# Performance work log

Hardware: AMD Instinct MI355X
Metric: run time of the kernel (lower is better)

## Reference

```python
import jax, jax.numpy as jnp
import numpy as np

EPS = 1e-5
NUM_HEADS = 8
KEY_DIM = 16
D = 64  # attn_ratio * key_dim


def conv1x1_bn(x, w, g, b, m, v):
    # x: (B, Cin, H, W), w: (Cout, Cin); eval-mode BatchNorm over channel dim
    y = jnp.einsum('bchw,oc->bohw', x, w)
    scale = (g * jax.lax.rsqrt(v + EPS))[None, :, None, None]
    shift = (b - g * m * jax.lax.rsqrt(v + EPS))[None, :, None, None]
    return y * scale + shift


def setup_inputs() -> dict:
    key = jax.random.key(0)
    ks = jax.random.split(key, 22)
    dim, nh_kd, dh = 384, 128, 512
    f = jax.random.normal
    u = jax.random.uniform
    return {
        'x': f(ks[0], (2, dim, 56, 56), jnp.float32),
        'wq': f(ks[1], (nh_kd, dim), jnp.float32) * 0.05,
        'qg': u(ks[2], (nh_kd,), jnp.float32), 'qb': f(ks[3], (nh_kd,)) * 0.1,
        'qm': f(ks[4], (nh_kd,)) * 0.1, 'qv': u(ks[5], (nh_kd,)) + 0.5,
        'wk': f(ks[6], (nh_kd, dim), jnp.float32) * 0.05,
        'kg': u(ks[7], (nh_kd,), jnp.float32), 'kb': f(ks[8], (nh_kd,)) * 0.1,
        'km': f(ks[9], (nh_kd,)) * 0.1, 'kvv': u(ks[10], (nh_kd,)) + 0.5,
        'wv': f(ks[11], (dh, dim), jnp.float32) * 0.05,
        'vg': u(ks[12], (dh,), jnp.float32), 'vb': f(ks[13], (dh,)) * 0.1,
        'vm': f(ks[14], (dh,)) * 0.1, 'vvv': u(ks[15], (dh,)) + 0.5,
        'wp': f(ks[16], (dim, dh), jnp.float32) * 0.05,
        'pg': u(ks[17], (dim,), jnp.float32), 'pb': f(ks[18], (dim,)) * 0.1,
        'pm': f(ks[19], (dim,)) * 0.1, 'pvv': u(ks[20], (dim,)) + 0.5,
    }


def reference(x, wq, qg, qb, qm, qv, wk, kg, kb, km, kvv,
              wv, vg, vb, vm, vvv, wp, pg, pb, pm, pvv):
    B, C, H, W = x.shape
    N = H * W
    h, kd, d = NUM_HEADS, KEY_DIM, D
    # (B, h, N, kd)
    qq = conv1x1_bn(x, wq, qg, qb, qm, qv).reshape(B, h, kd, N).transpose(0, 1, 3, 2)
    # (B, h, kd, N)
    kk = conv1x1_bn(x, wk, kg, kb, km, kvv).reshape(B, h, kd, N)
    # (B, h, N, d)
    vv = conv1x1_bn(x, wv, vg, vb, vm, vvv).reshape(B, h, d, N).transpose(0, 1, 3, 2)
    # NOTE: original forward does NOT apply self.scale
    attn = jax.nn.softmax(jnp.matmul(qq, kk), axis=-1)  # (B, h, N, N)
    xx = jnp.matmul(attn, vv)                            # (B, h, N, d)
    xx = xx.transpose(0, 1, 3, 2).reshape(B, h * d, H, W)
    xx = jax.nn.relu(xx)
    return conv1x1_bn(xx, wp, pg, pb, pm, pvv)
```

## Files before the change

kernel.cpp:

```cpp
#include <hip/hip_runtime.h>
#include <hip/hip_bf16.h>

#define B_   2
#define CIN  384
#define NPIX 3136
#define NH   8
#define KD   16
#define DHEAD 64
#define NHKD 128
#define QKW  256
#define DHD  512
#define EPSW 1e-5f

typedef __attribute__((ext_vector_type(8))) short vshort8;
typedef __attribute__((ext_vector_type(4))) short vshort4;
typedef __attribute__((ext_vector_type(4))) float vfloat4;

static __device__ __forceinline__ float bf2f(short s) {
    unsigned int u = ((unsigned int)(unsigned short)s) << 16;
    return __builtin_bit_cast(float, u);
}
static __device__ __forceinline__ short f2bf(float f) {
    unsigned int u = __builtin_bit_cast(unsigned int, f);
    unsigned int lsb = (u >> 16) & 1u;
    u += 0x7fffu + lsb;
    return (short)(u >> 16);
}
static __device__ __forceinline__ float pget(const void* p, int i, int f32) {
    return f32 ? ((const float*)p)[i] : bf2f(((const short*)p)[i]);
}

__global__ void detect_dtype(const unsigned short* __restrict__ x, int* __restrict__ flag) {
    int lane = threadIdx.x & 63;
    int cnt = 0;
#pragma unroll
    for (int j = 0; j < 8; j++) {
        int e = (x[(lane * 8 + j) * 2] >> 7) & 0xFF;
        cnt += (e >= 0xC0);
    }
    cnt += __shfl_xor(cnt, 1);
    cnt += __shfl_xor(cnt, 2);
    cnt += __shfl_xor(cnt, 4);
    cnt += __shfl_xor(cnt, 8);
    cnt += __shfl_xor(cnt, 16);
    cnt += __shfl_xor(cnt, 32);
    if (threadIdx.x == 0) *flag = (cnt >= 16) ? 1 : 0;
}

__global__ __launch_bounds__(256) void convert_and_bn(
    const void* __restrict__ wq, const void* __restrict__ wk,
    const void* __restrict__ wv, const void* __restrict__ wp,
    short* __restrict__ wB,
    const void* qg, const void* qb, const void* qm, const void* qv,
    const void* kg, const void* kb, const void* km, const void* kv,
    const void* vg, const void* vb, const void* vm, const void* vv,
    const void* pg, const void* pb, const void* pm, const void* pv,
    float* __restrict__ scA, float* __restrict__ shA,
    const int* __restrict__ flag)
{
    int f32 = *flag;
    int i = blockIdx.x * 256 + threadIdx.x;
    {
        const void* src; int j;
        if (i < 49152)       { src = wq; j = i; }
        else if (i < 98304)  { src = wk; j = i - 49152; }
        else if (i < 294912) { src = wv; j = i - 98304; }
        else                 { src = wp; j = i - 294912; }
        wB[i] = f32 ? f2bf(((const float*)src)[j]) : ((const short*)src)[j];
    }
    if (i < 1152) {
        const void *g, *bb, *mn, *vr; int j;
        if (i < 128)      { g = qg; bb = qb; mn = qm; vr = qv; j = i; }
        else if (i < 256) { g = kg; bb = kb; mn = km; vr = kv; j = i - 128; }
        else if (i < 768) { g = vg; bb = vb; mn = vm; vr = vv; j = i - 256; }
        else              { g = pg; bb = pb; mn = pm; vr = pv; j = i - 768; }
        float iv = rsqrtf(pget(vr, j, f32) + EPSW);
        float s = pget(g, j, f32) * iv;
        scA[i] = s;
        shA[i] = pget(bb, j, f32) - pget(mn, j, f32) * s;
    }
}

__global__ __launch_bounds__(256) void transpose_k(const void* __restrict__ x,
                                                   short* __restrict__ xT,
                                                   const int* __restrict__ flag) {
    __shared__ short tile[32][33];
    int f32 = *flag;
    int b = blockIdx.z, n0 = blockIdx.x * 32, c0 = blockIdx.y * 32;
    int t = threadIdx.x;
    int r = t >> 3, q4 = (t & 7) * 4;
    size_t off = ((size_t)b * CIN + c0 + r) * NPIX + n0 + q4;
    if (f32) {
        float4 v = *(const float4*)((const float*)x + off);
        tile[r][q4 + 0] = f2bf(v.x);
        tile[r][q4 + 1] = f2bf(v.y);
        tile[r][q4 + 2] = f2bf(v.z);
        tile[r][q4 + 3] = f2bf(v.w);
    } else {
        vshort4 v = *(const vshort4*)((const short*)x + off);
#pragma unroll
        for (int i = 0; i < 4; i++) tile[r][q4 + i] = v[i];
    }
    __syncthreads();
    vshort4 o;
#pragma unroll
    for (int i = 0; i < 4; i++) o[i] = tile[q4 + i][r];
    *(vshort4*)(xT + ((size_t)b * NPIX + n0 + r) * CIN + c0 + q4) = o;
}

__global__ __launch_bounds__(256) void gemm_bt_bn(
    const short* __restrict__ A, long sAb,
    const short* __restrict__ Bt, long sBb,
    void* __restrict__ C, long sCb,
    const float* __restrict__ sc, const float* __restrict__ sh,
    int Nb, int K, int bnPerRow, int finalOut,
    const int* __restrict__ flag)
{
    __shared__ __attribute__((aligned(16))) short Al[64 * 72];
    __shared__ __attribute__((aligned(16))) short Bl[64 * 72];
    int f32 = finalOut ? *flag : 0;
    int b = blockIdx.z;
    const short* Ab = A + (size_t)b * sAb;
    const short* Bb = Bt + (size_t)b * sBb;
    size_t cbase = (size_t)b * sCb;
    int m0 = blockIdx.x * 64, n0 = blockIdx.y * 64;
    int t = threadIdx.x, lane = t & 63, w = t >> 6, m = lane & 15, quad = lane >> 4;
    int srow = t >> 2, scol = (t & 3) * 16;
    const short* ag = Ab + (size_t)(m0 + srow) * K + scol;
    const short* bg = Bb + (size_t)(n0 + srow) * K + scol;
    vfloat4 acc[4];
#pragma unroll
    for (int i = 0; i < 4; i++) acc[i] = (vfloat4){0.f, 0.f, 0.f, 0.f};

    for (int k0 = 0; k0 < K; k0 += 64) {
        vshort8 a0 = *(const vshort8*)(ag + k0);
        vshort8 a1 = *(const vshort8*)(ag + k0 + 8);
        vshort8 b0 = *(const vshort8*)(bg + k0);
        vshort8 b1 = *(const vshort8*)(bg + k0 + 8);
        __syncthreads();
        *(vshort8*)&Al[srow * 72 + scol] = a0;
        *(vshort8*)&Al[srow * 72 + scol + 8] = a1;
        *(vshort8*)&Bl[srow * 72 + scol] = b0;
        *(vshort8*)&Bl[srow * 72 + scol + 8] = b1;
        __syncthreads();
#pragma unroll
        for (int kk = 0; kk < 2; kk++) {
            vshort8 af = *(const vshort8*)&Al[(w * 16 + m) * 72 + kk * 32 + quad * 8];
#pragma unroll
            for (int nc = 0; nc < 4; nc++) {
                vshort8 bf = *(const vshort8*)&Bl[(nc * 16 + m) * 72 + kk * 32 + quad * 8];
                acc[nc] = __builtin_amdgcn_mfma_f32_16x16x32_bf16(af, bf, acc[nc], 0, 0, 0);
            }
        }
    }

#pragma unroll
    for (int nc = 0; nc < 4; nc++) {
        int col = n0 + nc * 16 + m;
        float scc = bnPerRow ? 0.f : sc[col];
        float shc = bnPerRow ? 0.f : sh[col];
#pragma unroll
        for (int r = 0; r < 4; r++) {
            int row = m0 + w * 16 + quad * 4 + r;
            float s2 = bnPerRow ? sc[row] : scc;
            float h2 = bnPerRow ? sh[row] : shc;
            float val = s2 * acc[nc][r] + h2;
            size_t idx = cbase + (size_t)row * Nb + col;
            if (finalOut && f32) ((float*)C)[idx] = val;
            else                 ((short*)C)[idx] = f2bf(val);
        }
    }
}

__global__ __launch_bounds__(256) void attn_kernel(
    const short* __restrict__ QKt, const short* __restrict__ V,
    short* __restrict__ xx)
{
    __shared__ __attribute__((aligned(16))) short Kl[2][64 * 40];
    __shared__ __attribute__((aligned(16))) short Vl[2][64 * 72];
    __shared__ __attribute__((aligned(16))) short Pl[64 * 72];
    int bh = blockIdx.y, b = bh >> 3, h = bh & 7;
    int q0 = blockIdx.x * 64;
    int t = threadIdx.x, lane = t & 63, w = t >> 6, m = lane & 15, quad = lane >> 4;

    {
        int key = t >> 2;
        int z = 16 + (t & 3) * 4;
        *(vshort4*)&Kl[0][key * 40 + z] = (vshort4){0, 0, 0, 0};
        *(vshort4*)&Kl[1][key * 40 + z] = (vshort4){0, 0, 0, 0};
    }

    int q = q0 + w * 16 + m;
    vshort8 aq;
    if (quad < 2) {
        aq = *(const vshort8*)(QKt + ((size_t)b * NPIX + q) * QKW + h * KD + quad * 8);
    } else {
        aq = (vshort8){0, 0, 0, 0, 0, 0, 0, 0};
    }

    vfloat4 o[4], o4;
#pragma unroll
    for (int i = 0; i < 4; i++) o[i] = (vfloat4){0.f, 0.f, 0.f, 0.f};
    o4 = (vfloat4){0.f, 0.f, 0.f, 0.f};

    int skey = t >> 2, skd = (t & 3) * 4;
    const short* kgp = QKt + (size_t)b * NPIX * QKW + NHKD + h * KD + skd;
    int vrow = t >> 2, vcol = (t & 3) * 16;
    const short* vgp = V + ((size_t)(b * DHD) + h * DHEAD + vrow) * NPIX + vcol;
    const vfloat4 zero4 = (vfloat4){0.f, 0.f, 0.f, 0.f};
    const short one_bf = (short)0x3F80;
    const vshort8 ones = {one_bf, one_bf, one_bf, one_bf, one_bf, one_bf, one_bf, one_bf};

    {
        vshort4 kstg = *(const vshort4*)(kgp + (size_t)skey * QKW);
        vshort8 v0 = *(const vshort8*)(vgp);
        vshort8 v1 = *(const vshort8*)(vgp + 8);
        *(vshort4*)&Kl[0][skey * 40 + skd] = kstg;
        *(vshort8*)&Vl[0][vrow * 72 + vcol] = v0;
        *(vshort8*)&Vl[0][vrow * 72 + vcol + 8] = v1;
    }
    __syncthreads();

    for (int it = 0; it < NPIX / 64; ++it) {
        int cur = it & 1, nxt = cur ^ 1;
        int k0 = it * 64;
        int more = (it + 1) < (NPIX / 64);
        vshort4 kstg; vshort8 v0, v1;
        if (more) {
            kstg = *(const vshort4*)(kgp + (size_t)(k0 + 64 + skey) * QKW);
            v0 = *(const vshort8*)(vgp + k0 + 64);
            v1 = *(const vshort8*)(vgp + k0 + 72);
        }

        vfloat4 s[4];
#pragma unroll
        for (int c = 0; c < 4; c++) {
            vshort8 ak = *(const vshort8*)&Kl[cur][(c * 16 + m) * 40 + quad * 8];
            s[c] = __builtin_amdgcn_mfma_f32_16x16x32_bf16(ak, aq, zero4, 0, 0, 0);
        }

        short* pw = &Pl[(w * 16 + m) * 72];
#pragma unroll
        for (int c = 0; c < 4; c++) {
            vshort4 pv;
#pragma unroll
            for (int r = 0; r < 4; r++) {
                float p = __expf(s[c][r]);
                pv[r] = (short)(__builtin_bit_cast(unsigned int, p) >> 16);
            }
            *(vshort4*)&pw[c * 16 + quad * 4] = pv;
        }

#pragma unroll
        for (int kc = 0; kc < 2; kc++) {
            vshort8 ap = *(const vshort8*)&Pl[(w * 16 + m) * 72 + kc * 32 + quad * 8];
#pragma unroll
            for (int dc = 0; dc < 4; dc++) {
                vshort8 bv = *(const vshort8*)&Vl[cur][(dc * 16 + m) * 72 + kc * 32 + quad * 8];
                o[dc] = __builtin_amdgcn_mfma_f32_16x16x32_bf16(ap, bv, o[dc], 0, 0, 0);
            }
            o4 = __builtin_amdgcn_mfma_f32_16x16x32_bf16(ap, ones, o4, 0, 0, 0);
        }

        if (more) {
            *(vshort4*)&Kl[nxt][skey * 40 + skd] = kstg;
            *(vshort8*)&Vl[nxt][vrow * 72 + vcol] = v0;
            *(vshort8*)&Vl[nxt][vrow * 72 + vcol + 8] = v1;
        }
        __syncthreads();
    }

#pragma unroll
    for (int r = 0; r < 4; r++) {
        float inv = 1.0f / o4[r];
        int qrow = q0 + w * 16 + quad * 4 + r;
        size_t base = ((size_t)b * NPIX + qrow) * DHD + h * DHEAD + m;
#pragma unroll
        for (int dc = 0; dc < 4; dc++) {
            float val = o[dc][r] * inv;
            val = fmaxf(val, 0.0f);
            xx[base + dc * 16] = f2bf(val);
        }
    }
}

extern "C" void kernel_launch(void* const* d_in, const int* in_sizes, int n_in,
                              void* d_out, int out_size, void* d_ws, size_t ws_size,
                              hipStream_t stream) {
    const void* x  = d_in[0];
    const void* wq = d_in[1];
    const void* qg = d_in[2];  const void* qb = d_in[3];
    const void* qm = d_in[4];  const void* qv = d_in[5];
    const void* wk = d_in[6];
    const void* kg = d_in[7];  const void* kb = d_in[8];
    const void* km = d_in[9];  const void* kv = d_in[10];
    const void* wv = d_in[11];
    const void* vg = d_in[12]; const void* vb = d_in[13];
    const void* vm = d_in[14]; const void* vv = d_in[15];
    const void* wp = d_in[16];
    const void* pg = d_in[17]; const void* pb = d_in[18];
    const void* pm = d_in[19]; const void* pv = d_in[20];

    short* xT  = (short*)d_ws;
    short* wB  = xT + (size_t)B_ * NPIX * CIN;
    short* wqkB = wB;
    short* wvB  = wB + 98304;
    short* wpB  = wB + 294912;
    short* QKt = wB + 491520;
    short* Vb  = QKt + (size_t)B_ * NPIX * QKW;
    short* xx  = Vb + (size_t)B_ * DHD * NPIX;
    float* scA = (float*)(xx + (size_t)B_ * NPIX * DHD);
    float* shA = scA + 1152;
    int* flag  = (int*)(shA + 1152);

    detect_dtype<<<1, 64, 0, stream>>>((const unsigned short*)x, flag);
    convert_and_bn<<<491520 / 256, 256, 0, stream>>>(
        wq, wk, wv, wp, wB,
        qg, qb, qm, qv, kg, kb, km, kv,
        vg, vb, vm, vv, pg, pb, pm, pv, scA, shA, flag);
    transpose_k<<<dim3(NPIX / 32, CIN / 32, B_), 256, 0, stream>>>(x, xT, flag);

    gemm_bt_bn<<<dim3(NPIX / 64, QKW / 64, B_), 256, 0, stream>>>(
        xT, (long)NPIX * CIN, wqkB, 0, QKt, (long)NPIX * QKW,
        scA, shA, QKW, CIN, 0, 0, flag);
    gemm_bt_bn<<<dim3(DHD / 64, NPIX / 64, B_), 256, 0, stream>>>(
        wvB, 0, xT, (long)NPIX * CIN, Vb, (long)DHD * NPIX,
        scA + 256, shA + 256, NPIX, CIN, 1, 0, flag);

    attn_kernel<<<dim3(NPIX / 64, B_ * NH), 256, 0, stream>>>(QKt, Vb, xx);

    gemm_bt_bn<<<dim3(CIN / 64, NPIX / 64, B_), 256, 0, stream>>>(
        wpB, 0, xx, (long)NPIX * DHD, d_out, (long)CIN * NPIX,
        scA + 768, shA + 768, NPIX, DHD, 1, 1, flag);
}
```

Baseline: 214.0 us.

## Fuse prep and projection launches, switch attention to 32x32 MFMA tiles

Folds dtype detection, weight conversion, BN folding and the input transpose into one prep kernel, and merges the QK and V projection GEMMs into a single launch, cutting the launch count from seven to four. The attention kernel now uses 128-thread blocks with two waves of 32 queries each and 32x32x16 bf16 MFMAs. This removes the zero-padded K tile the old kernel needed to fit the 16-wide key dim into 16x16x32. Every block now recomputes the dtype detection redundantly, and fewer waves per block may lower latency hiding in attention.

```diff
diff --git a/kernel.cpp b/kernel.cpp
--- a/kernel.cpp
+++ b/kernel.cpp
@@ -15,6 +15,7 @@
 typedef __attribute__((ext_vector_type(8))) short vshort8;
 typedef __attribute__((ext_vector_type(4))) short vshort4;
 typedef __attribute__((ext_vector_type(4))) float vfloat4;
+typedef __attribute__((ext_vector_type(16))) float vfloat16;
 
 static __device__ __forceinline__ float bf2f(short s) {
     unsigned int u = ((unsigned int)(unsigned short)s) << 16;
@@ -30,64 +31,59 @@
     return f32 ? ((const float*)p)[i] : bf2f(((const short*)p)[i]);
 }
 
-__global__ void detect_dtype(const unsigned short* __restrict__ x, int* __restrict__ flag) {
+static __device__ __forceinline__ int detect_f32(const unsigned short* x) {
     int lane = threadIdx.x & 63;
-    int cnt = 0;
+    bool big = false;
 #pragma unroll
     for (int j = 0; j < 8; j++) {
         int e = (x[(lane * 8 + j) * 2] >> 7) & 0xFF;
-        cnt += (e >= 0xC0);
-    }
-    cnt += __shfl_xor(cnt, 1);
-    cnt += __shfl_xor(cnt, 2);
-    cnt += __shfl_xor(cnt, 4);
-    cnt += __shfl_xor(cnt, 8);
-    cnt += __shfl_xor(cnt, 16);
-    cnt += __shfl_xor(cnt, 32);
-    if (threadIdx.x == 0) *flag = (cnt >= 16) ? 1 : 0;
-}
-
-__global__ __launch_bounds__(256) void convert_and_bn(
+        big = big || (e >= 0xC0);
+    }
+    unsigned long long bal = __ballot(big);
+    return __popcll(bal) >= 32;
+}
+
+__global__ __launch_bounds__(256) void prep_kernel(
+    const void* __restrict__ x,
     const void* __restrict__ wq, const void* __restrict__ wk,
     const void* __restrict__ wv, const void* __restrict__ wp,
-    short* __restrict__ wB,
+    short* __restrict__ wB, short* __restrict__ xT,
     const void* qg, const void* qb, const void* qm, const void* qv,
     const void* kg, const void* kb, const void* km, const void* kv,
     const void* vg, const void* vb, const void* vm, const void* vv,
     const void* pg, const void* pb, const void* pm, const void* pv,
-    float* __restrict__ scA, float* __restrict__ shA,
-    const int* __restrict__ flag)
-{
-    int f32 = *flag;
-    int i = blockIdx.x * 256 + threadIdx.x;
-    {
+    float* __restrict__ scA, float* __restrict__ shA)
+{
+    __shared__ short tile[32][33];
+    int f32 = detect_f32((const unsigned short*)x);
+    int id = blockIdx.x;
+    int t = threadIdx.x;
+
+    if (id < 1920) {
+        int i = id * 256 + t;
         const void* src; int j;
         if (i < 49152)       { src = wq; j = i; }
         else if (i < 98304)  { src = wk; j = i - 49152; }
         else if (i < 294912) { src = wv; j = i - 98304; }
         else                 { src = wp; j = i - 294912; }
         wB[i] = f32 ? f2bf(((const float*)src)[j]) : ((const short*)src)[j];
-    }
-    if (i < 1152) {
-        const void *g, *bb, *mn, *vr; int j;
-        if (i < 128)      { g = qg; bb = qb; mn = qm; vr = qv; j = i; }
-        else if (i < 256) { g = kg; bb = kb; mn = km; vr = kv; j = i - 128; }
-        else if (i < 768) { g = vg; bb = vb; mn = vm; vr = vv; j = i - 256; }
-        else              { g = pg; bb = pb; mn = pm; vr = pv; j = i - 768; }
-        float iv = rsqrtf(pget(vr, j, f32) + EPSW);
-        float s = pget(g, j, f32) * iv;
-        scA[i] = s;
-        shA[i] = pget(bb, j, f32) - pget(mn, j, f32) * s;
-    }
-}
-
-__global__ __launch_bounds__(256) void transpose_k(const void* __restrict__ x,
-                                                   short* __restrict__ xT,
-                                                   const int* __restrict__ flag) {
-    __shared__ short tile[32][33];
-    int f32 = *flag;
-    int b = blockIdx.z, n0 = blockIdx.x * 32, c0 = blockIdx.y * 32;
-    int t = threadIdx.x;
+        if (i < 1152) {
+            const void *g, *bb, *mn, *vr;
+            if (i < 128)      { g = qg; bb = qb; mn = qm; vr = qv; j = i; }
+            else if (i < 256) { g = kg; bb = kb; mn = km; vr = kv; j = i - 128; }
+            else if (i < 768) { g = vg; bb = vb; mn = vm; vr = vv; j = i - 256; }
+            else              { g = pg; bb = pb; mn = pm; vr = pv; j = i - 768; }
+            float iv = rsqrtf(pget(vr, j, f32) + EPSW);
+            float s = pget(g, j, f32) * iv;
+            scA[i] = s;
+            shA[i] = pget(bb, j, f32) - pget(mn, j, f32) * s;
+        }
+        return;
+    }
+
+    int tid2 = id - 1920;
+    int b = tid2 / 1176, rr = tid2 % 1176;
+    int n0 = (rr % 98) * 32, c0 = (rr / 98) * 32;
     int r = t >> 3, q4 = (t & 7) * 4;
     size_t off = ((size_t)b * CIN + c0 + r) * NPIX + n0 + q4;
     if (f32) {
@@ -108,26 +104,17 @@
     *(vshort4*)(xT + ((size_t)b * NPIX + n0 + r) * CIN + c0 + q4) = o;
 }
 
-__global__ __launch_bounds__(256) void gemm_bt_bn(
-    const short* __restrict__ A, long sAb,
-    const short* __restrict__ Bt, long sBb,
-    void* __restrict__ C, long sCb,
+static __device__ __forceinline__ void gemm_body(
+    short* Al, short* Bl,
+    const short* __restrict__ A, const short* __restrict__ Bt,
+    void* __restrict__ C, size_t coff, int m0, int n0,
     const float* __restrict__ sc, const float* __restrict__ sh,
-    int Nb, int K, int bnPerRow, int finalOut,
-    const int* __restrict__ flag)
-{
-    __shared__ __attribute__((aligned(16))) short Al[64 * 72];
-    __shared__ __attribute__((aligned(16))) short Bl[64 * 72];
-    int f32 = finalOut ? *flag : 0;
-    int b = blockIdx.z;
-    const short* Ab = A + (size_t)b * sAb;
-    const short* Bb = Bt + (size_t)b * sBb;
-    size_t cbase = (size_t)b * sCb;
-    int m0 = blockIdx.x * 64, n0 = blockIdx.y * 64;
+    int Nb, int K, int bnPerRow, int finalOut, int f32)
+{
     int t = threadIdx.x, lane = t & 63, w = t >> 6, m = lane & 15, quad = lane >> 4;
     int srow = t >> 2, scol = (t & 3) * 16;
-    const short* ag = Ab + (size_t)(m0 + srow) * K + scol;
-    const short* bg = Bb + (size_t)(n0 + srow) * K + scol;
+    const short* ag = A + (size_t)(m0 + srow) * K + scol;
+    const short* bg = Bt + (size_t)(n0 + srow) * K + scol;
     vfloat4 acc[4];
 #pragma unroll
     for (int i = 0; i < 4; i++) acc[i] = (vfloat4){0.f, 0.f, 0.f, 0.f};
@@ -165,122 +152,143 @@
             float s2 = bnPerRow ? sc[row] : scc;
             float h2 = bnPerRow ? sh[row] : shc;
             float val = s2 * acc[nc][r] + h2;
-            size_t idx = cbase + (size_t)row * Nb + col;
+            size_t idx = coff + (size_t)row * Nb + col;
             if (finalOut && f32) ((float*)C)[idx] = val;
             else                 ((short*)C)[idx] = f2bf(val);
         }
     }
 }
 
-__global__ __launch_bounds__(256) void attn_kernel(
+__global__ __launch_bounds__(256) void proj_kernel(
+    const short* __restrict__ xT, const short* __restrict__ wqkB,
+    const short* __restrict__ wvB, short* __restrict__ QKt,
+    short* __restrict__ Vb,
+    const float* __restrict__ scA, const float* __restrict__ shA)
+{
+    __shared__ __attribute__((aligned(16))) short Al[64 * 72];
+    __shared__ __attribute__((aligned(16))) short Bl[64 * 72];
+    int id = blockIdx.x;
+    if (id < 392) {
+        int b = id / 196, r = id % 196;
+        int m0 = (r % 49) * 64, n0 = (r / 49) * 64;
+        gemm_body(Al, Bl, xT + (size_t)b * NPIX * CIN, wqkB,
+                  QKt, (size_t)b * NPIX * QKW, m0, n0,
+                  scA, shA, QKW, CIN, 0, 0, 0);
+    } else {
+        id -= 392;
+        int b = id / 392, r = id % 392;
+        int m0 = (r % 8) * 64, n0 = (r / 8) * 64;
+        gemm_body(Al, Bl, wvB, xT + (size_t)b * NPIX * CIN,
+                  Vb, (size_t)b * DHD * NPIX, m0, n0,
+                  scA + 256, shA + 256, NPIX, CIN, 1, 0, 0);
+    }
+}
+
+__global__ __launch_bounds__(256) void pgemm_kernel(
+    const short* __restrict__ wpB, const short* __restrict__ xx,
+    void* __restrict__ out,
+    const float* __restrict__ scA, const float* __restrict__ shA,
+    const void* __restrict__ x)
+{
+    __shared__ __attribute__((aligned(16))) short Al[64 * 72];
+    __shared__ __attribute__((aligned(16))) short Bl[64 * 72];
+    int f32 = detect_f32((const unsigned short*)x);
+    int id = blockIdx.x;
+    int b = id / 294, r = id % 294;
+    int m0 = (r % 6) * 64, n0 = (r / 6) * 64;
+    gemm_body(Al, Bl, wpB, xx + (size_t)b * NPIX * DHD,
+              out, (size_t)b * CIN * NPIX, m0, n0,
+              scA + 768, shA + 768, NPIX, DHD, 1, 1, f32);
+}
+
+__global__ __launch_bounds__(128) void attn_kernel(
     const short* __restrict__ QKt, const short* __restrict__ V,
     short* __restrict__ xx)
 {
-    __shared__ __attribute__((aligned(16))) short Kl[2][64 * 40];
+    __shared__ __attribute__((aligned(16))) short Kl[2][64 * 16];
     __shared__ __attribute__((aligned(16))) short Vl[2][64 * 72];
     __shared__ __attribute__((aligned(16))) short Pl[64 * 72];
     int bh = blockIdx.y, b = bh >> 3, h = bh & 7;
     int q0 = blockIdx.x * 64;
-    int t = threadIdx.x, lane = t & 63, w = t >> 6, m = lane & 15, quad = lane >> 4;
-
-    {
-        int key = t >> 2;
-        int z = 16 + (t & 3) * 4;
-        *(vshort4*)&Kl[0][key * 40 + z] = (vshort4){0, 0, 0, 0};
-        *(vshort4*)&Kl[1][key * 40 + z] = (vshort4){0, 0, 0, 0};
-    }
-
-    int q = q0 + w * 16 + m;
-    vshort8 aq;
-    if (quad < 2) {
-        aq = *(const vshort8*)(QKt + ((size_t)b * NPIX + q) * QKW + h * KD + quad * 8);
-    } else {
-        aq = (vshort8){0, 0, 0, 0, 0, 0, 0, 0};
-    }
-
-    vfloat4 o[4], o4;
-#pragma unroll
-    for (int i = 0; i < 4; i++) o[i] = (vfloat4){0.f, 0.f, 0.f, 0.f};
-    o4 = (vfloat4){0.f, 0.f, 0.f, 0.f};
-
-    int skey = t >> 2, skd = (t & 3) * 4;
-    const short* kgp = QKt + (size_t)b * NPIX * QKW + NHKD + h * KD + skd;
-    int vrow = t >> 2, vcol = (t & 3) * 16;
-    const short* vgp = V + ((size_t)(b * DHD) + h * DHEAD + vrow) * NPIX + vcol;
-    const vfloat4 zero4 = (vfloat4){0.f, 0.f, 0.f, 0.f};
+    int t = threadIdx.x, lane = t & 63, w = t >> 6;
+    int c31 = lane & 31, half = lane >> 5;
+
+    int q = q0 + w * 32 + c31;
+    vshort8 aq = *(const vshort8*)(QKt + ((size_t)b * NPIX + q) * QKW + h * KD + half * 8);
+
+    vfloat16 o0, o1, oL, z16;
+#pragma unroll
+    for (int i = 0; i < 16; i++) { o0[i] = 0.f; o1[i] = 0.f; oL[i] = 0.f; z16[i] = 0.f; }
+
+    int kkey = t >> 1, kofs = (t & 1) * 8;
+    const short* kgp = QKt + (size_t)b * NPIX * QKW + NHKD + h * KD + kofs;
+    int vd = t >> 1, vkh = (t & 1) * 32;
+    const short* vgp = V + ((size_t)(b * DHD) + h * DHEAD + vd) * NPIX + vkh;
     const short one_bf = (short)0x3F80;
     const vshort8 ones = {one_bf, one_bf, one_bf, one_bf, one_bf, one_bf, one_bf, one_bf};
 
-    {
-        vshort4 kstg = *(const vshort4*)(kgp + (size_t)skey * QKW);
-        vshort8 v0 = *(const vshort8*)(vgp);
-        vshort8 v1 = *(const vshort8*)(vgp + 8);
-        *(vshort4*)&Kl[0][skey * 40 + skd] = kstg;
-        *(vshort8*)&Vl[0][vrow * 72 + vcol] = v0;
-        *(vshort8*)&Vl[0][vrow * 72 + vcol + 8] = v1;
-    }
+    *(vshort8*)&Kl[0][kkey * 16 + kofs] = *(const vshort8*)(kgp + (size_t)kkey * QKW);
+#pragma unroll
+    for (int i = 0; i < 4; i++)
+        *(vshort8*)&Vl[0][vd * 72 + vkh + i * 8] = *(const vshort8*)(vgp + i * 8);
     __syncthreads();
 
     for (int it = 0; it < NPIX / 64; ++it) {
         int cur = it & 1, nxt = cur ^ 1;
         int k0 = it * 64;
-        int more = (it + 1) < (NPIX / 64);
-        vshort4 kstg; vshort8 v0, v1;
+        bool more = (it + 1) < (NPIX / 64);
+        vshort8 ks, vs[4];
         if (more) {
-            kstg = *(const vshort4*)(kgp + (size_t)(k0 + 64 + skey) * QKW);
-            v0 = *(const vshort8*)(vgp + k0 + 64);
-            v1 = *(const vshort8*)(vgp + k0 + 72);
-        }
-
-        vfloat4 s[4];
-#pragma unroll
-        for (int c = 0; c < 4; c++) {
-            vshort8 ak = *(const vshort8*)&Kl[cur][(c * 16 + m) * 40 + quad * 8];
-            s[c] = __builtin_amdgcn_mfma_f32_16x16x32_bf16(ak, aq, zero4, 0, 0, 0);
-        }
-
-        short* pw = &Pl[(w * 16 + m) * 72];
-#pragma unroll
-        for (int c = 0; c < 4; c++) {
-            vshort4 pv;
-#pragma unroll
-            for (int r = 0; r < 4; r++) {
-                float p = __expf(s[c][r]);
-                pv[r] = (short)(__builtin_bit_cast(unsigned int, p) >> 16);
+            ks = *(const vshort8*)(kgp + (size_t)(k0 + 64 + kkey) * QKW);
+#pragma unroll
+            for (int i = 0; i < 4; i++)
+                vs[i] = *(const vshort8*)(vgp + k0 + 64 + i * 8);
+        }
+
+        short* pw = &Pl[(w * 32 + c31) * 72];
+#pragma unroll
+        for (int kg = 0; kg < 2; kg++) {
+            vshort8 ak = *(const vshort8*)&Kl[cur][(kg * 32 + c31) * 16 + half * 8];
+            vfloat16 s = __builtin_amdgcn_mfma_f32_32x32x16_bf16(ak, aq, z16, 0, 0, 0);
+#pragma unroll
+            for (int rb = 0; rb < 4; rb++) {
+                vshort4 pv;
+#pragma unroll
+                for (int j = 0; j < 4; j++) {
+                    float p = __expf(s[rb * 4 + j]);
+                    pv[j] = (short)(__builtin_bit_cast(unsigned int, p) >> 16);
+                }
+                *(vshort4*)&pw[kg * 32 + half * 4 + rb * 8] = pv;
             }
-            *(vshort4*)&pw[c * 16 + quad * 4] = pv;
-        }
-
-#pragma unroll
-        for (int kc = 0; kc < 2; kc++) {
-            vshort8 ap = *(const vshort8*)&Pl[(w * 16 + m) * 72 + kc * 32 + quad * 8];
-#pragma unroll
-            for (int dc = 0; dc < 4; dc++) {
-                vshort8 bv = *(const vshort8*)&Vl[cur][(dc * 16 + m) * 72 + kc * 32 + quad * 8];
-                o[dc] = __builtin_amdgcn_mfma_f32_16x16x32_bf16(ap, bv, o[dc], 0, 0, 0);
-            }
-            o4 = __builtin_amdgcn_mfma_f32_16x16x32_bf16(ap, ones, o4, 0, 0, 0);
+        }
+
+#pragma unroll
+        for (int kc = 0; kc < 4; kc++) {
+            vshort8 ap  = *(const vshort8*)&Pl[(w * 32 + c31) * 72 + kc * 16 + half * 8];
+            vshort8 bv0 = *(const vshort8*)&Vl[cur][(c31) * 72 + kc * 16 + half * 8];
+            vshort8 bv1 = *(const vshort8*)&Vl[cur][(32 + c31) * 72 + kc * 16 + half * 8];
+            o0 = __builtin_amdgcn_mfma_f32_32x32x16_bf16(ap, bv0, o0, 0, 0, 0);
+            o1 = __builtin_amdgcn_mfma_f32_32x32x16_bf16(ap, bv1, o1, 0, 0, 0);
+            oL = __builtin_amdgcn_mfma_f32_32x32x16_bf16(ap, ones, oL, 0, 0, 0);
         }
 
         if (more) {
-            *(vshort4*)&Kl[nxt][skey * 40 + skd] = kstg;
-            *(vshort8*)&Vl[nxt][vrow * 72 + vcol] = v0;
-            *(vshort8*)&Vl[nxt][vrow * 72 + vcol + 8] = v1;
+            *(vshort8*)&Kl[nxt][kkey * 16 + kofs] = ks;
+#pragma unroll
+            for (int i = 0; i < 4; i++)
+                *(vshort8*)&Vl[nxt][vd * 72 + vkh + i * 8] = vs[i];
         }
         __syncthreads();
     }
 
 #pragma unroll
-    for (int r = 0; r < 4; r++) {
-        float inv = 1.0f / o4[r];
-        int qrow = q0 + w * 16 + quad * 4 + r;
-        size_t base = ((size_t)b * NPIX + qrow) * DHD + h * DHEAD + m;
-#pragma unroll
-        for (int dc = 0; dc < 4; dc++) {
-            float val = o[dc][r] * inv;
-            val = fmaxf(val, 0.0f);
-            xx[base + dc * 16] = f2bf(val);
-        }
+    for (int r = 0; r < 16; r++) {
+        int ql = (r & 3) + 8 * (r >> 2) + 4 * half;
+        int qrow = q0 + w * 32 + ql;
+        float inv = 1.0f / oL[r];
+        size_t base = ((size_t)b * NPIX + qrow) * DHD + h * DHEAD + c31;
+        xx[base]      = f2bf(fmaxf(o0[r] * inv, 0.f));
+        xx[base + 32] = f2bf(fmaxf(o1[r] * inv, 0.f));
     }
 }
 
@@ -311,25 +319,15 @@
     short* xx  = Vb + (size_t)B_ * DHD * NPIX;
     float* scA = (float*)(xx + (size_t)B_ * NPIX * DHD);
     float* shA = scA + 1152;
-    int* flag  = (int*)(shA + 1152);
-
-    detect_dtype<<<1, 64, 0, stream>>>((const unsigned short*)x, flag);
-    convert_and_bn<<<491520 / 256, 256, 0, stream>>>(
-        wq, wk, wv, wp, wB,
+
+    prep_kernel<<<4272, 256, 0, stream>>>(
+        x, wq, wk, wv, wp, wB, xT,
         qg, qb, qm, qv, kg, kb, km, kv,
-        vg, vb, vm, vv, pg, pb, pm, pv, scA, shA, flag);
-    transpose_k<<<dim3(NPIX / 32, CIN / 32, B_), 256, 0, stream>>>(x, xT, flag);
-
-    gemm_bt_bn<<<dim3(NPIX / 64, QKW / 64, B_), 256, 0, stream>>>(
-        xT, (long)NPIX * CIN, wqkB, 0, QKt, (long)NPIX * QKW,
-        scA, shA, QKW, CIN, 0, 0, flag);
-    gemm_bt_bn<<<dim3(DHD / 64, NPIX / 64, B_), 256, 0, stream>>>(
-        wvB, 0, xT, (long)NPIX * CIN, Vb, (long)DHD * NPIX,
-        scA + 256, shA + 256, NPIX, CIN, 1, 0, flag);
-
-    attn_kernel<<<dim3(NPIX / 64, B_ * NH), 256, 0, stream>>>(QKt, Vb, xx);
-
-    gemm_bt_bn<<<dim3(CIN / 64, NPIX / 64, B_), 256, 0, stream>>>(
-        wpB, 0, xx, (long)NPIX * DHD, d_out, (long)CIN * NPIX,
-        scA + 768, shA + 768, NPIX, DHD, 1, 1, flag);
-}
+        vg, vb, vm, vv, pg, pb, pm, pv, scA, shA);
+
+    proj_kernel<<<1176, 256, 0, stream>>>(xT, wqkB, wvB, QKt, Vb, scA, shA);
+
+    attn_kernel<<<dim3(NPIX / 64, B_ * NH), 128, 0, stream>>>(QKt, Vb, xx);
+
+    pgemm_kernel<<<588, 256, 0, stream>>>(wpB, xx, d_out, scA, shA, x);
+}
```

Result: faster. 197.2 us (-7.9%).
